# Kernel tuning notes

Measured on AMD Instinct MI355X. Metric: run time of the kernel, lower is better.

## Reference

```python
import jax
jax.config.update("jax_enable_x64", True)  # hashing needs true int64 like torch
import jax.numpy as jnp
import numpy as np
import itertools

N_DIM = 3
N_ENTRIES = 4194304  # 2**22
N_FEATURE = 4
BATCH = 2097152  # 2**21 sample points
GRIDS = np.array([128.0, 128.0, 128.0], dtype=np.float32)
PRIMES = np.array([1, 19349663, 83492791], dtype=np.int64)
BIT_TABLE = np.array(list(itertools.product([0, 1], repeat=N_DIM)), dtype=np.int32)  # (2^D, D)


def setup_inputs() -> dict:
    key = jax.random.key(0)
    k1, k2 = jax.random.split(key)
    position = jax.random.uniform(k1, (BATCH, N_DIM), dtype=jnp.float32)  # in [0,1)^D
    hash_table = (jax.random.uniform(k2, (N_ENTRIES, N_FEATURE), dtype=jnp.float32) - 0.5) * 2e-4
    return {"position": position, "hash_table": hash_table}


def reference(position, hash_table):
    grids = jnp.asarray(GRIDS)           # (D,) float32
    bit = jnp.asarray(BIT_TABLE)         # (2^D, D) int32
    primes = jnp.asarray(PRIMES)         # (D,) int64

    # findGrid: lower corner on the integer grid
    lower = jnp.floor(position * grids).astype(jnp.int32)          # (B, D)
    # all 2^D corners of the enclosing cell
    corner = lower[:, None, :] + bit[None, :, :]                    # (B, 2^D, D)

    # spatial hash: XOR of index*prime, reduced mod table size each step (as torch does)
    h = jnp.zeros(corner.shape[:-1], dtype=jnp.int64)               # (B, 2^D)
    for i in range(N_DIM):
        h = jnp.bitwise_xor(h, corner[..., i].astype(jnp.int64) * primes[i]) % N_ENTRIES

    corner_value = hash_table[h]                                    # (B, 2^D, F) gather

    # multilinear interpolation coefficients (faithful to source's weight assignment)
    lower_f = lower / grids                                         # (B, D)
    upper_f = (lower + 1) / grids                                   # (B, D)
    size = (upper_f - lower_f)[0]                                   # (D,) uniform cell size
    coef = jnp.stack([(position - lower_f) / size,
                      (upper_f - position) / size], axis=-1)        # (B, D, 2)
    # weight per corner = prod over dims of the bit-selected coefficient
    w = jnp.prod(coef[:, jnp.arange(N_DIM)[None, :], bit], axis=2)  # (B, 2^D)

    return jnp.sum(corner_value * w[..., None], axis=1)             # (B, F)
```

## Files before the change

### kernel.cpp

```cpp
#include <hip/hip_runtime.h>
#include <stdint.h>


#define HASH_MASK 0x3FFFFFu
#define P1 19349663u
#define P2 83492791u
#define NBUCK 64
#define PPT 16
#define K3_BLOCK 256
#define PPB (K3_BLOCK * PPT)

__device__ __forceinline__ uint32_t bucket_of(float px, float py, float pz) {
    uint32_t bx = ((uint32_t)(int)floorf(px * 128.0f)) >> 5;
    uint32_t by = ((uint32_t)(int)floorf(py * 128.0f)) >> 5;
    uint32_t bz = ((uint32_t)(int)floorf(pz * 128.0f)) >> 5;
    return (bx << 4) | (by << 2) | bz;
}

__device__ __forceinline__ float4 interp_point(float px, float py, float pz,
                                               const float* __restrict__ table) {
    int lx = (int)floorf(px * 128.0f);
    int ly = (int)floorf(py * 128.0f);
    int lz = (int)floorf(pz * 128.0f);

    const float inv = 1.0f / 128.0f;
    float w0x = (px - (float)lx * inv) * 128.0f;
    float w1x = ((float)(lx + 1) * inv - px) * 128.0f;
    float w0y = (py - (float)ly * inv) * 128.0f;
    float w1y = ((float)(ly + 1) * inv - py) * 128.0f;
    float w0z = (pz - (float)lz * inv) * 128.0f;
    float w1z = ((float)(lz + 1) * inv - pz) * 128.0f;

    uint32_t hx0 = (uint32_t)lx;
    uint32_t hx1 = (uint32_t)(lx + 1);
    uint32_t hy0 = (uint32_t)ly * P1;
    uint32_t hy1 = (uint32_t)(ly + 1) * P1;
    uint32_t hz0 = (uint32_t)lz * P2;
    uint32_t hz1 = (uint32_t)(lz + 1) * P2;

    float acc0 = 0.f, acc1 = 0.f, acc2 = 0.f, acc3 = 0.f;
#pragma unroll
    for (int c = 0; c < 8; ++c) {
        int bx = (c >> 2) & 1;
        int by = (c >> 1) & 1;
        int bz = c & 1;
        uint32_t h = ((bx ? hx1 : hx0) ^ (by ? hy1 : hy0) ^ (bz ? hz1 : hz0)) & HASH_MASK;
        const float4 v = *reinterpret_cast<const float4*>(table + (size_t)h * 4);
        float w = ((bx ? w1x : w0x) * (by ? w1y : w0y)) * (bz ? w1z : w0z);
        acc0 += v.x * w;
        acc1 += v.y * w;
        acc2 += v.z * w;
        acc3 += v.w * w;
    }
    return make_float4(acc0, acc1, acc2, acc3);
}

__global__ __launch_bounds__(K3_BLOCK) void hist_kernel(
    const float* __restrict__ pos, uint32_t* __restrict__ hist, int batch)
{
    __shared__ uint32_t h[NBUCK];
    int tid = threadIdx.x;
    size_t start = (size_t)blockIdx.x * PPB;
    if (tid < NBUCK) h[tid] = 0;
    __syncthreads();
#pragma unroll
    for (int k = 0; k < PPT; ++k) {
        size_t i = start + (size_t)k * K3_BLOCK + tid;
        if (i < (size_t)batch) {
            float px = pos[3 * i + 0];
            float py = pos[3 * i + 1];
            float pz = pos[3 * i + 2];
            atomicAdd(&h[bucket_of(px, py, pz)], 1u);
        }
    }
    __syncthreads();
    if (tid < NBUCK && h[tid]) atomicAdd(&hist[tid], h[tid]);
}

__global__ __launch_bounds__(64) void scan_kernel(
    const uint32_t* __restrict__ hist, uint32_t* __restrict__ cursor)
{
    int t = threadIdx.x;
    uint32_t v = hist[t];
    uint32_t inc = v;
    for (int off = 1; off < 64; off <<= 1) {
        uint32_t n = __shfl_up(inc, off);
        if (t >= off) inc += n;
    }
    cursor[t] = inc - v;
}

__global__ __launch_bounds__(K3_BLOCK) void scatter_kernel(
    const float* __restrict__ pos, uint32_t* __restrict__ cursor,
    float4* __restrict__ sorted, int batch)
{
    __shared__ float4 staged[PPB];
    __shared__ uint32_t h[NBUCK], lbase[NBUCK], gbase[NBUCK], lcur[NBUCK];
    int tid = threadIdx.x;
    size_t start = (size_t)blockIdx.x * PPB;

    if (tid < NBUCK) h[tid] = 0;
    __syncthreads();

    float px[PPT], py[PPT], pz[PPT];
    uint32_t bb[PPT];
#pragma unroll
    for (int k = 0; k < PPT; ++k) {
        size_t i = start + (size_t)k * K3_BLOCK + tid;
        px[k] = pos[3 * i + 0];
        py[k] = pos[3 * i + 1];
        pz[k] = pos[3 * i + 2];
        bb[k] = bucket_of(px[k], py[k], pz[k]);
        atomicAdd(&h[bb[k]], 1u);
    }
    __syncthreads();

    if (tid < NBUCK) {
        uint32_t v = h[tid];
        uint32_t inc = v;
        for (int off = 1; off < 64; off <<= 1) {
            uint32_t n = __shfl_up(inc, off);
            if (tid >= off) inc += n;
        }
        uint32_t excl = inc - v;
        lbase[tid] = excl;
        lcur[tid] = excl;
        gbase[tid] = atomicAdd(&cursor[tid], v);
    }
    __syncthreads();

#pragma unroll
    for (int k = 0; k < PPT; ++k) {
        size_t i = start + (size_t)k * K3_BLOCK + tid;
        uint32_t slot = atomicAdd(&lcur[bb[k]], 1u);
        staged[slot] = make_float4(px[k], py[k], pz[k], __uint_as_float((uint32_t)i));
    }
    __syncthreads();

#pragma unroll
    for (int k = 0; k < PPT; ++k) {
        int j = k * K3_BLOCK + tid;
        float4 s = staged[j];
        uint32_t b = bucket_of(s.x, s.y, s.z);
        sorted[gbase[b] + ((uint32_t)j - lbase[b])] = s;
    }
}

__global__ __launch_bounds__(256) void interp_scatter_kernel(
    const float4* __restrict__ sorted, const float* __restrict__ table,
    float4* __restrict__ out4, int batch, int nwg)
{
    int bid = blockIdx.x;
    int q = nwg >> 3;
    int swz = (bid & 7) * q + (bid >> 3);
    int i = swz * 256 + threadIdx.x;
    if (i >= batch) return;

    float4 s = sorted[i];
    float4 r = interp_point(s.x, s.y, s.z, table);
    uint32_t orig = __float_as_uint(s.w);
    out4[orig] = r;
}

__global__ __launch_bounds__(256) void interp_direct_kernel(
    const float* __restrict__ pos, const float* __restrict__ table,
    float4* __restrict__ out4, int batch)
{
    int i = blockIdx.x * 256 + threadIdx.x;
    if (i >= batch) return;
    float px = pos[3 * (size_t)i + 0];
    float py = pos[3 * (size_t)i + 1];
    float pz = pos[3 * (size_t)i + 2];
    out4[i] = interp_point(px, py, pz, table);
}

extern "C" void kernel_launch(void* const* d_in, const int* in_sizes, int n_in,
                              void* d_out, int out_size, void* d_ws, size_t ws_size,
                              hipStream_t stream) {
    const float* pos   = (const float*)d_in[0];
    const float* table = (const float*)d_in[1];
    float4* out4 = (float4*)d_out;

    int batch = in_sizes[0] / 3;
    int blocks256 = (batch + 255) / 256;

    size_t sorted_off = 512;
    size_t need = sorted_off + (size_t)batch * 16;

    bool exact = (batch % PPB == 0) && ((blocks256 & 7) == 0);
    if (ws_size < need || !exact) {
        interp_direct_kernel<<<blocks256, 256, 0, stream>>>(pos, table, out4, batch);
        return;
    }

    uint32_t* hist   = (uint32_t*)d_ws;
    uint32_t* cursor = (uint32_t*)((char*)d_ws + 256);
    float4*   sorted = (float4*)((char*)d_ws + sorted_off);

    int sblocks = batch / PPB;

    hipMemsetAsync(hist, 0, NBUCK * sizeof(uint32_t), stream);
    hist_kernel<<<sblocks, K3_BLOCK, 0, stream>>>(pos, hist, batch);
    scan_kernel<<<1, 64, 0, stream>>>(hist, cursor);
    scatter_kernel<<<sblocks, K3_BLOCK, 0, stream>>>(pos, cursor, sorted, batch);
    interp_scatter_kernel<<<blocks256, 256, 0, stream>>>(sorted, table, out4, batch, blocks256);
}
```

Baseline: 124.4 us.

## Add per-bucket fine Morton subsort before interpolation gather

```diff
diff --git a/kernel.cpp b/kernel.cpp
--- a/kernel.cpp
+++ b/kernel.cpp
@@ -6,6 +6,7 @@
 #define P1 19349663u
 #define P2 83492791u
 #define NBUCK 64
+#define FBINS 512
 #define PPT 16
 #define K3_BLOCK 256
 #define PPB (K3_BLOCK * PPT)
@@ -15,6 +16,17 @@
     uint32_t by = ((uint32_t)(int)floorf(py * 128.0f)) >> 5;
     uint32_t bz = ((uint32_t)(int)floorf(pz * 128.0f)) >> 5;
     return (bx << 4) | (by << 2) | bz;
+}
+
+__device__ __forceinline__ uint32_t spread3(uint32_t v) {
+    return (v & 1u) | ((v & 2u) << 2) | ((v & 4u) << 4);
+}
+
+__device__ __forceinline__ uint32_t fine_bin(float px, float py, float pz) {
+    uint32_t cx = (((uint32_t)(int)floorf(px * 128.0f)) >> 2) & 7u;
+    uint32_t cy = (((uint32_t)(int)floorf(py * 128.0f)) >> 2) & 7u;
+    uint32_t cz = (((uint32_t)(int)floorf(pz * 128.0f)) >> 2) & 7u;
+    return (spread3(cx) << 2) | (spread3(cy) << 1) | spread3(cz);
 }
 
 __device__ __forceinline__ float4 interp_point(float px, float py, float pz,
@@ -146,6 +158,47 @@
     }
 }
 
+__global__ __launch_bounds__(1024) void subsort_kernel(
+    const float4* __restrict__ sorted, const uint32_t* __restrict__ cursor,
+    float4* __restrict__ sorted2)
+{
+    __shared__ uint32_t hist[FBINS];
+    __shared__ uint32_t scanb[FBINS];
+    int b = blockIdx.x;
+    int tid = threadIdx.x;
+    uint32_t start = (b == 0) ? 0u : cursor[b - 1];
+    uint32_t end = cursor[b];
+    uint32_t n = end - start;
+
+    if (tid < FBINS) hist[tid] = 0;
+    __syncthreads();
+
+    for (uint32_t j = tid; j < n; j += 1024) {
+        float4 s = sorted[start + j];
+        atomicAdd(&hist[fine_bin(s.x, s.y, s.z)], 1u);
+    }
+    __syncthreads();
+
+    uint32_t v = (tid < FBINS) ? hist[tid] : 0u;
+    if (tid < FBINS) scanb[tid] = v;
+    __syncthreads();
+    for (int off = 1; off < FBINS; off <<= 1) {
+        uint32_t add = 0;
+        if (tid < FBINS && tid >= off) add = scanb[tid - off];
+        __syncthreads();
+        if (tid < FBINS) scanb[tid] += add;
+        __syncthreads();
+    }
+    if (tid < FBINS) hist[tid] = scanb[tid] - v;
+    __syncthreads();
+
+    for (uint32_t j = tid; j < n; j += 1024) {
+        float4 s = sorted[start + j];
+        uint32_t slot = atomicAdd(&hist[fine_bin(s.x, s.y, s.z)], 1u);
+        sorted2[start + slot] = s;
+    }
+}
+
 __global__ __launch_bounds__(256) void interp_scatter_kernel(
     const float4* __restrict__ sorted, const float* __restrict__ table,
     float4* __restrict__ out4, int batch, int nwg)
@@ -184,18 +237,21 @@
     int batch = in_sizes[0] / 3;
     int blocks256 = (batch + 255) / 256;
 
-    size_t sorted_off = 512;
-    size_t need = sorted_off + (size_t)batch * 16;
+    size_t sorted_off  = 512;
+    size_t sorted2_off = sorted_off + (size_t)batch * 16;
+    size_t need1 = sorted_off + (size_t)batch * 16;
+    size_t need2 = sorted2_off + (size_t)batch * 16;
 
     bool exact = (batch % PPB == 0) && ((blocks256 & 7) == 0);
-    if (ws_size < need || !exact) {
+    if (ws_size < need1 || !exact) {
         interp_direct_kernel<<<blocks256, 256, 0, stream>>>(pos, table, out4, batch);
         return;
     }
 
-    uint32_t* hist   = (uint32_t*)d_ws;
-    uint32_t* cursor = (uint32_t*)((char*)d_ws + 256);
-    float4*   sorted = (float4*)((char*)d_ws + sorted_off);
+    uint32_t* hist    = (uint32_t*)d_ws;
+    uint32_t* cursor  = (uint32_t*)((char*)d_ws + 256);
+    float4*   sorted  = (float4*)((char*)d_ws + sorted_off);
+    float4*   sorted2 = (float4*)((char*)d_ws + sorted2_off);
 
     int sblocks = batch / PPB;
 
@@ -203,5 +259,11 @@
     hist_kernel<<<sblocks, K3_BLOCK, 0, stream>>>(pos, hist, batch);
     scan_kernel<<<1, 64, 0, stream>>>(hist, cursor);
     scatter_kernel<<<sblocks, K3_BLOCK, 0, stream>>>(pos, cursor, sorted, batch);
-    interp_scatter_kernel<<<blocks256, 256, 0, stream>>>(sorted, table, out4, batch, blocks256);
-}
+
+    if (ws_size >= need2) {
+        subsort_kernel<<<NBUCK, 1024, 0, stream>>>(sorted, cursor, sorted2);
+        interp_scatter_kernel<<<blocks256, 256, 0, stream>>>(sorted2, table, out4, batch, blocks256);
+    } else {
+        interp_scatter_kernel<<<blocks256, 256, 0, stream>>>(sorted, table, out4, batch, blocks256);
+    }
+}
```

New measurement: 141.3 us. +13.5%, slower.
